# Performance work log

Measured on AMD Instinct MI355X. Metric: run time of the kernel, lower is better.

Reference implementation:

```python
import jax, jax.numpy as jnp
import numpy as np

WINDOW_SIZE = 11
SIGMA = 1.5
C1 = 0.01 ** 2
C2 = 0.03 ** 2


def _gaussian_window(channel, dtype):
    # 1D gaussian, normalized, then outer product -> 2D window, expanded per channel
    xs = np.arange(WINDOW_SIZE) - WINDOW_SIZE // 2
    g = np.exp(-(xs.astype(np.float64) ** 2) / (2.0 * SIGMA ** 2))
    g = (g / g.sum()).astype(np.float32)
    w2d = np.outer(g, g)  # [ws, ws]
    w = np.broadcast_to(w2d[None, None], (channel, 1, WINDOW_SIZE, WINDOW_SIZE))
    return jnp.asarray(w, dtype=dtype)


def _depthwise_conv(img, window, channel):
    pad = WINDOW_SIZE // 2
    return jax.lax.conv_general_dilated(
        img, window,
        window_strides=(1, 1),
        padding=[(pad, pad), (pad, pad)],
        dimension_numbers=('NCHW', 'OIHW', 'NCHW'),
        feature_group_count=channel)


def setup_inputs() -> dict:
    key = jax.random.key(0)
    k1, k2 = jax.random.split(key)
    shape = (16, 3, 512, 512)
    x = jax.random.uniform(k1, shape, dtype=jnp.float32)
    y = jax.random.uniform(k2, shape, dtype=jnp.float32)
    return {"x": x, "y": y}


def reference(x, y):
    channel = x.shape[-3]
    window = _gaussian_window(channel, x.dtype)

    mu1 = _depthwise_conv(x, window, channel)
    mu2 = _depthwise_conv(y, window, channel)
    mu1_sq = mu1 * mu1
    mu2_sq = mu2 * mu2
    mu1_mu2 = mu1 * mu2
    sigma1_sq = _depthwise_conv(x * x, window, channel) - mu1_sq
    sigma2_sq = _depthwise_conv(y * y, window, channel) - mu2_sq
    sigma12 = _depthwise_conv(x * y, window, channel) - mu1_mu2

    ssim_map = ((2.0 * mu1_mu2 + C1) * (2.0 * sigma12 + C2)) / (
        (mu1_sq + mu2_sq + C1) * (sigma1_sq + sigma2_sq + C2))
    # DSSIM = 1 - mean(ssim)
    return 1.0 - jnp.mean(ssim_map)
```

## Files before the change

kernel.cpp:

```cpp
#include <hip/hip_runtime.h>


typedef _Float16 half8 __attribute__((ext_vector_type(8)));
typedef _Float16 half4v __attribute__((ext_vector_type(4)));
typedef __fp16 pk16 __attribute__((ext_vector_type(2)));
typedef float f32x4 __attribute__((ext_vector_type(4)));
typedef float f32x8 __attribute__((ext_vector_type(8)));

#define IMG_W   512
#define IMG_H   512
#define NPLANES 48
#define BR      16
#define TP      40
#define GRX     (IMG_H / BR)
#define NBLK    (GRX * NPLANES)

__global__ __launch_bounds__(256, 3)
void dssim_main(const float* __restrict__ xin, const float* __restrict__ yin,
                float* __restrict__ partial) {
    __shared__ _Float16 ldsT[4][4][16][TP];
    __shared__ float wpart[4];

    const int t    = threadIdx.x;
    const int lane = t & 63;
    const int wid  = t >> 6;
    const int bn   = lane & 15;
    const int jg   = lane >> 4;
    const int swz  = (bn & 8) << 1;
    const int r0   = blockIdx.x * BR;
    const size_t pbase = (size_t)blockIdx.y * (IMG_W * IMG_H);
    const float* __restrict__ xp = xin + pbase;
    const float* __restrict__ yp = yin + pbase;

    float ginv;
    {
        float s = 0.f;
#pragma unroll
        for (int i = 0; i < 11; ++i) {
            float d = (float)(i - 5);
            s += expf(-(d * d) * (1.0f / 4.5f));
        }
        ginv = 1.0f / s;
    }

    half8 whF, wvF;
#pragma unroll
    for (int j = 0; j < 8; ++j) {
        const int k = 8 * jg + j;
        const int dh = k - bn - 3;
        const int dv = k - bn;
        float wh = 0.f, wv = 0.f;
        if (dh >= 0 && dh < 11) {
            const float d = (float)(dh - 5);
            wh = ginv * expf(-(d * d) * (1.0f / 4.5f));
        }
        if (dv >= 0 && dv < 11) {
            const float d = (float)(dv - 5);
            wv = ginv * expf(-(d * d) * (1.0f / 4.5f));
        }
        whF[j] = (_Float16)wh;
        wvF[j] = (_Float16)wv;
    }

    const int gr0 = r0 - 5 + bn;
    const bool rowok0 = (gr0 >= 0) && (gr0 < IMG_H);
    const int gr1 = r0 + 11 + bn;
    const bool rowok1 = (bn < 10) && (gr1 < IMG_H);
    const size_t row0 = (size_t)(rowok0 ? gr0 : 0) * IMG_W;
    const size_t row1 = (size_t)(rowok1 ? gr1 : 0) * IMG_W;

    const f32x8 z8 = {0.f, 0.f, 0.f, 0.f, 0.f, 0.f, 0.f, 0.f};
    const f32x4 zf = {0.f, 0.f, 0.f, 0.f};
    const float C1 = 0.0001f, C2 = 0.0009f;
    float lsum = 0.f;

    f32x8 xs0, ys0, xs1, ys1;

#define LOADI(ii)                                                           \
    {                                                                       \
        const int col = (((wid + 4 * (ii)) << 4) + 8 * jg) - 8;             \
        const bool colok = (col >= 0) && (col < IMG_W);                     \
        const size_t co = (size_t)(colok ? col : 0);                        \
        const bool ok0 = colok && rowok0, ok1 = colok && rowok1;            \
        xs0 = ok0 ? *(const f32x8*)(xp + row0 + co) : z8;                   \
        ys0 = ok0 ? *(const f32x8*)(yp + row0 + co) : z8;                   \
        xs1 = ok1 ? *(const f32x8*)(xp + row1 + co) : z8;                   \
        ys1 = ok1 ? *(const f32x8*)(yp + row1 + co) : z8;                   \
    }

#define HCOMPI(ii)                                                          \
    {                                                                       \
        _Pragma("unroll")                                                   \
        for (int rt = 0; rt < 2; ++rt) {                                    \
            const f32x8 xv = rt ? xs1 : xs0;                                \
            const f32x8 yv = rt ? ys1 : ys0;                                \
            half8 aU, aW;                                                   \
            _Pragma("unroll")                                               \
            for (int d = 0; d < 4; ++d) {                                   \
                const pk16 pu = __builtin_amdgcn_cvt_pkrtz(                 \
                    xv[2 * d] + yv[2 * d], xv[2 * d + 1] + yv[2 * d + 1]);  \
                const pk16 pw = __builtin_amdgcn_cvt_pkrtz(                 \
                    xv[2 * d] - yv[2 * d], xv[2 * d + 1] - yv[2 * d + 1]);  \
                aU[2 * d] = (_Float16)pu[0]; aU[2 * d + 1] = (_Float16)pu[1]; \
                aW[2 * d] = (_Float16)pw[0]; aW[2 * d + 1] = (_Float16)pw[1]; \
            }                                                               \
            const half8 aU2 = aU * aU;                                      \
            const half8 aW2 = aW * aW;                                      \
            const f32x4 cU  = __builtin_amdgcn_mfma_f32_16x16x32_f16(aU,  whF, zf, 0, 0, 0); \
            const f32x4 cW  = __builtin_amdgcn_mfma_f32_16x16x32_f16(aW,  whF, zf, 0, 0, 0); \
            const f32x4 cU2 = __builtin_amdgcn_mfma_f32_16x16x32_f16(aU2, whF, zf, 0, 0, 0); \
            const f32x4 cW2 = __builtin_amdgcn_mfma_f32_16x16x32_f16(aW2, whF, zf, 0, 0, 0); \
            half4v hU, hW, hU2, hW2;                                        \
            _Pragma("unroll")                                               \
            for (int q = 0; q < 2; ++q) {                                   \
                const pk16 p0 = __builtin_amdgcn_cvt_pkrtz(cU[2*q],  cU[2*q+1]);  \
                const pk16 p1 = __builtin_amdgcn_cvt_pkrtz(cW[2*q],  cW[2*q+1]);  \
                const pk16 p2 = __builtin_amdgcn_cvt_pkrtz(cU2[2*q], cU2[2*q+1]); \
                const pk16 p3 = __builtin_amdgcn_cvt_pkrtz(cW2[2*q], cW2[2*q+1]); \
                hU[2*q]  = (_Float16)p0[0]; hU[2*q+1]  = (_Float16)p0[1];   \
                hW[2*q]  = (_Float16)p1[0]; hW[2*q+1]  = (_Float16)p1[1];   \
                hU2[2*q] = (_Float16)p2[0]; hU2[2*q+1] = (_Float16)p2[1];   \
                hW2[2*q] = (_Float16)p3[0]; hW2[2*q+1] = (_Float16)p3[1];   \
            }                                                               \
            const int kk = (16 * rt + 4 * jg) ^ swz;                        \
            *(half4v*)&ldsT[wid][0][bn][kk] = hU;                           \
            *(half4v*)&ldsT[wid][1][bn][kk] = hW;                           \
            *(half4v*)&ldsT[wid][2][bn][kk] = hU2;                          \
            *(half4v*)&ldsT[wid][3][bn][kk] = hW2;                          \
        }                                                                   \
    }

#define VBLURI(ii)                                                          \
    {                                                                       \
        const int kb = (8 * jg) ^ swz;                                      \
        const half8 aTU  = *(const half8*)&ldsT[wid][0][bn][kb];            \
        const half8 aTW  = *(const half8*)&ldsT[wid][1][bn][kb];            \
        const half8 aTU2 = *(const half8*)&ldsT[wid][2][bn][kb];            \
        const half8 aTW2 = *(const half8*)&ldsT[wid][3][bn][kb];            \
        const f32x4 accU = __builtin_amdgcn_mfma_f32_16x16x32_f16(aTU,  wvF, zf, 0, 0, 0); \
        const f32x4 accW = __builtin_amdgcn_mfma_f32_16x16x32_f16(aTW,  wvF, zf, 0, 0, 0); \
        const f32x4 accP = __builtin_amdgcn_mfma_f32_16x16x32_f16(aTU2, wvF, zf, 0, 0, 0); \
        const f32x4 accQ = __builtin_amdgcn_mfma_f32_16x16x32_f16(aTW2, wvF, zf, 0, 0, 0); \
        _Pragma("unroll")                                                   \
        for (int q = 0; q < 4; ++q) {                                       \
            const float U = accU[q], W = accW[q];                           \
            const float P = accP[q], Q = accQ[q];                           \
            const float U2 = U * U, W2 = W * W;                             \
            const float A = 0.5f * (U2 + W2);                               \
            const float B = 0.5f * (U2 - W2);                               \
            const float den2 = fmaf(0.5f, P + Q, -A) + C2;                  \
            const float num2 = fmaf(0.5f, P - Q, -B) + C2;                  \
            lsum += (B + C1) * num2 * __builtin_amdgcn_rcpf((A + C1) * den2); \
        }                                                                   \
    }

    LOADI(0);
    HCOMPI(0);
#pragma unroll
    for (int i = 0; i < 8; ++i) {
        if (i + 1 < 8) LOADI(i + 1);
        VBLURI(i);
        if (i + 1 < 8) HCOMPI(i + 1);
    }

#pragma unroll
    for (int off = 32; off >= 1; off >>= 1)
        lsum += __shfl_down(lsum, off, 64);
    if (lane == 0) wpart[wid] = lsum;
    __syncthreads();
    if (t == 0) {
        partial[(size_t)blockIdx.y * GRX + blockIdx.x] =
            wpart[0] + wpart[1] + wpart[2] + wpart[3];
    }
}

__global__ __launch_bounds__(256)
void dssim_final(const float* __restrict__ partial, float* __restrict__ out) {
    __shared__ double wsum[4];
    double s = 0.0;
    for (int i = threadIdx.x; i < NBLK; i += 256) s += (double)partial[i];
#pragma unroll
    for (int off = 32; off >= 1; off >>= 1)
        s += __shfl_down(s, off, 64);
    if ((threadIdx.x & 63) == 0) wsum[threadIdx.x >> 6] = s;
    __syncthreads();
    if (threadIdx.x == 0) {
        const double tot = wsum[0] + wsum[1] + wsum[2] + wsum[3];
        out[0] = (float)(1.0 - tot / 12582912.0);
    }
}

extern "C" void kernel_launch(void* const* d_in, const int* in_sizes, int n_in,
                              void* d_out, int out_size, void* d_ws, size_t ws_size,
                              hipStream_t stream) {
    const float* x = (const float*)d_in[0];
    const float* y = (const float*)d_in[1];
    float* out = (float*)d_out;
    float* partial = (float*)d_ws;

    dim3 grid(GRX, NPLANES);
    dim3 block(256);
    dssim_main<<<grid, block, 0, stream>>>(x, y, partial);
    dssim_final<<<1, block, 0, stream>>>(partial, out);
}
```

Measured before the change: 48.28 us.

## Process two column tiles per step with double-buffered LDS and simplified loads

Each wave now loads and horizontally blurs two column tiles per pipeline step, using a second LDS buffer slot, so more global loads are in flight while the vertical-blur MFMAs run. Column bounds checks are replaced with fixed base pointers, and only the first and last lanes get a shifted address that is then zeroed. Row masking runs only in edge blocks. LDS row padding shrinks from 40 to 36 so the doubled buffer fits. The cost is higher register pressure from eight live f32x8 load vectors, which may hurt occupancy at the launch bound of 3 blocks, and the new padding may change LDS bank conflicts.

```diff
diff --git a/kernel.cpp b/kernel.cpp
--- a/kernel.cpp
+++ b/kernel.cpp
@@ -11,14 +11,14 @@
 #define IMG_H   512
 #define NPLANES 48
 #define BR      16
-#define TP      40
+#define TP      36
 #define GRX     (IMG_H / BR)
 #define NBLK    (GRX * NPLANES)
 
 __global__ __launch_bounds__(256, 3)
 void dssim_main(const float* __restrict__ xin, const float* __restrict__ yin,
                 float* __restrict__ partial) {
-    __shared__ _Float16 ldsT[4][4][16][TP];
+    __shared__ _Float16 ldsT[4][2][4][16][TP];
     __shared__ float wpart[4];
 
     const int t    = threadIdx.x;
@@ -28,6 +28,7 @@
     const int jg   = lane >> 4;
     const int swz  = (bn & 8) << 1;
     const int r0   = blockIdx.x * BR;
+    const bool edge = (blockIdx.x == 0) || (blockIdx.x == GRX - 1);
     const size_t pbase = (size_t)blockIdx.y * (IMG_W * IMG_H);
     const float* __restrict__ xp = xin + pbase;
     const float* __restrict__ yp = yin + pbase;
@@ -69,31 +70,47 @@
     const size_t row0 = (size_t)(rowok0 ? gr0 : 0) * IMG_W;
     const size_t row1 = (size_t)(rowok1 ? gr1 : 0) * IMG_W;
 
+    const int cb = (wid << 4) + (jg << 3) - 8;
+    const float* bx0 = xp + row0 + cb;
+    const float* by0 = yp + row0 + cb;
+    const float* bx1 = xp + row1 + cb;
+    const float* by1 = yp + row1 + cb;
+
     const f32x8 z8 = {0.f, 0.f, 0.f, 0.f, 0.f, 0.f, 0.f, 0.f};
     const f32x4 zf = {0.f, 0.f, 0.f, 0.f};
     const float C1 = 0.0001f, C2 = 0.0009f;
     float lsum = 0.f;
 
-    f32x8 xs0, ys0, xs1, ys1;
-
-#define LOADI(ii)                                                           \
+    f32x8 xa0, ya0, xa1, ya1, xb0, yb0, xb1, yb1;
+
+#define LOADP(m, XS0, YS0, XS1, YS1)                                        \
     {                                                                       \
-        const int col = (((wid + 4 * (ii)) << 4) + 8 * jg) - 8;             \
-        const bool colok = (col >= 0) && (col < IMG_W);                     \
-        const size_t co = (size_t)(colok ? col : 0);                        \
-        const bool ok0 = colok && rowok0, ok1 = colok && rowok1;            \
-        xs0 = ok0 ? *(const f32x8*)(xp + row0 + co) : z8;                   \
-        ys0 = ok0 ? *(const f32x8*)(yp + row0 + co) : z8;                   \
-        xs1 = ok1 ? *(const f32x8*)(xp + row1 + co) : z8;                   \
-        ys1 = ok1 ? *(const f32x8*)(yp + row1 + co) : z8;                   \
-    }
-
-#define HCOMPI(ii)                                                          \
+        int fix = 0;                                                        \
+        if ((m) == 0) fix = (wid == 0 && jg == 0) ? 8 : 0;                  \
+        if ((m) == 7) fix = (wid == 3 && jg == 3) ? -8 : 0;                 \
+        const int off = 64 * (m);                                           \
+        XS0 = *(const f32x8*)(bx0 + off + fix);                             \
+        YS0 = *(const f32x8*)(by0 + off + fix);                             \
+        XS1 = *(const f32x8*)(bx1 + off + fix);                             \
+        YS1 = *(const f32x8*)(by1 + off + fix);                             \
+        if ((m) == 0) {                                                     \
+            if (wid == 0 && jg == 0) { XS0 = z8; YS0 = z8; XS1 = z8; YS1 = z8; } \
+        }                                                                   \
+        if ((m) == 7) {                                                     \
+            if (wid == 3 && jg == 3) { XS0 = z8; YS0 = z8; XS1 = z8; YS1 = z8; } \
+        }                                                                   \
+        if (edge) {                                                         \
+            if (!rowok0) { XS0 = z8; YS0 = z8; }                            \
+            if (!rowok1) { XS1 = z8; YS1 = z8; }                            \
+        }                                                                   \
+    }
+
+#define HCOMP(s, XS0, YS0, XS1, YS1)                                        \
     {                                                                       \
         _Pragma("unroll")                                                   \
         for (int rt = 0; rt < 2; ++rt) {                                    \
-            const f32x8 xv = rt ? xs1 : xs0;                                \
-            const f32x8 yv = rt ? ys1 : ys0;                                \
+            const f32x8 xv = rt ? XS1 : XS0;                                \
+            const f32x8 yv = rt ? YS1 : YS0;                                \
             half8 aU, aW;                                                   \
             _Pragma("unroll")                                               \
             for (int d = 0; d < 4; ++d) {                                   \
@@ -123,20 +140,20 @@
                 hW2[2*q] = (_Float16)p3[0]; hW2[2*q+1] = (_Float16)p3[1];   \
             }                                                               \
             const int kk = (16 * rt + 4 * jg) ^ swz;                        \
-            *(half4v*)&ldsT[wid][0][bn][kk] = hU;                           \
-            *(half4v*)&ldsT[wid][1][bn][kk] = hW;                           \
-            *(half4v*)&ldsT[wid][2][bn][kk] = hU2;                          \
-            *(half4v*)&ldsT[wid][3][bn][kk] = hW2;                          \
-        }                                                                   \
-    }
-
-#define VBLURI(ii)                                                          \
+            *(half4v*)&ldsT[wid][s][0][bn][kk] = hU;                        \
+            *(half4v*)&ldsT[wid][s][1][bn][kk] = hW;                        \
+            *(half4v*)&ldsT[wid][s][2][bn][kk] = hU2;                       \
+            *(half4v*)&ldsT[wid][s][3][bn][kk] = hW2;                       \
+        }                                                                   \
+    }
+
+#define VBLUR(s)                                                            \
     {                                                                       \
         const int kb = (8 * jg) ^ swz;                                      \
-        const half8 aTU  = *(const half8*)&ldsT[wid][0][bn][kb];            \
-        const half8 aTW  = *(const half8*)&ldsT[wid][1][bn][kb];            \
-        const half8 aTU2 = *(const half8*)&ldsT[wid][2][bn][kb];            \
-        const half8 aTW2 = *(const half8*)&ldsT[wid][3][bn][kb];            \
+        const half8 aTU  = *(const half8*)&ldsT[wid][s][0][bn][kb];         \
+        const half8 aTW  = *(const half8*)&ldsT[wid][s][1][bn][kb];         \
+        const half8 aTU2 = *(const half8*)&ldsT[wid][s][2][bn][kb];         \
+        const half8 aTW2 = *(const half8*)&ldsT[wid][s][3][bn][kb];         \
         const f32x4 accU = __builtin_amdgcn_mfma_f32_16x16x32_f16(aTU,  wvF, zf, 0, 0, 0); \
         const f32x4 accW = __builtin_amdgcn_mfma_f32_16x16x32_f16(aTW,  wvF, zf, 0, 0, 0); \
         const f32x4 accP = __builtin_amdgcn_mfma_f32_16x16x32_f16(aTU2, wvF, zf, 0, 0, 0); \
@@ -154,13 +171,22 @@
         }                                                                   \
     }
 
-    LOADI(0);
-    HCOMPI(0);
-#pragma unroll
-    for (int i = 0; i < 8; ++i) {
-        if (i + 1 < 8) LOADI(i + 1);
-        VBLURI(i);
-        if (i + 1 < 8) HCOMPI(i + 1);
+    LOADP(0, xa0, ya0, xa1, ya1);
+    LOADP(1, xb0, yb0, xb1, yb1);
+    HCOMP(0, xa0, ya0, xa1, ya1);
+    HCOMP(1, xb0, yb0, xb1, yb1);
+#pragma unroll
+    for (int i2 = 0; i2 < 4; ++i2) {
+        if (i2 < 3) {
+            LOADP(2 * i2 + 2, xa0, ya0, xa1, ya1);
+            LOADP(2 * i2 + 3, xb0, yb0, xb1, yb1);
+        }
+        VBLUR(0);
+        VBLUR(1);
+        if (i2 < 3) {
+            HCOMP(0, xa0, ya0, xa1, ya1);
+            HCOMP(1, xb0, yb0, xb1, yb1);
+        }
     }
 
 #pragma unroll
```

New measurement: 49.21 us. No clear change (+1.9%).
